# Kernel tuning notes

Measured on AMD Instinct MI355X. Metric: run time of the kernel, lower is better.

The kernel has to match this reference:

```python
import jax, jax.numpy as jnp
import numpy as np

N_NODES = 40000      # batch of group nodes
DEGREE = 32          # neighbors (members) per node
NUM_USERS = 100000
NUM_GROUPS = 50000
EMBED_DIM = 64


def setup_inputs() -> dict:
    key = jax.random.key(0)
    ks = jax.random.split(key, 8)
    E = N_NODES * DEGREE
    d = EMBED_DIM
    return {
        "nodes": jax.random.randint(ks[0], (N_NODES,), 0, NUM_GROUPS),
        "neigh_idx": jax.random.randint(ks[1], (E,), 0, NUM_USERS),
        # edge i belongs to node segment_ids[i]; sorted, DEGREE edges per node
        "segment_ids": jnp.repeat(jnp.arange(N_NODES), DEGREE),
        "u2e_weight": jax.random.normal(ks[2], (NUM_USERS, d), jnp.float32) * 0.02,
        "g2e_weight": jax.random.normal(ks[3], (NUM_GROUPS, d), jnp.float32) * 0.02,
        "att1_w": jax.random.normal(ks[4], (d, 2 * d), jnp.float32) * (1.0 / np.sqrt(2 * d)),
        "att1_b": jnp.zeros((d,), jnp.float32),
        "att2_w": jax.random.normal(ks[5], (d, d), jnp.float32) * (1.0 / np.sqrt(d)),
        "att2_b": jnp.zeros((d,), jnp.float32),
        "att3_w": jax.random.normal(ks[6], (1, d), jnp.float32) * (1.0 / np.sqrt(d)),
        "att3_b": jnp.zeros((1,), jnp.float32),
    }


def _segment_softmax(logits, seg, num_segments):
    # numerically stable softmax within each node's neighbor segment
    m = jax.ops.segment_max(logits, seg, num_segments=num_segments)
    a = jnp.exp(logits - m[seg])
    s = jax.ops.segment_sum(a, seg, num_segments=num_segments)
    return a / s[seg]


def reference(nodes, neigh_idx, segment_ids, u2e_weight, g2e_weight,
              att1_w, att1_b, att2_w, att2_b, att3_w, att3_b):
    e_u = u2e_weight[neigh_idx]                 # [E, d] member embeddings
    g_rep = g2e_weight[nodes][segment_ids]      # [E, d] group query broadcast per edge
    x = jnp.concatenate([e_u, g_rep], axis=-1)  # [E, 2d]
    h = jax.nn.relu(x @ att1_w.T + att1_b)      # [E, d] (dropout inactive at eval)
    h = jax.nn.relu(h @ att2_w.T + att2_b)      # [E, d]
    logits = (h @ att3_w.T + att3_b)[:, 0]      # [E]
    att = _segment_softmax(logits, segment_ids, N_NODES)  # [E]
    # attention-weighted aggregation of member embeddings per node
    return jax.ops.segment_sum(att[:, None] * e_u, segment_ids, num_segments=N_NODES)  # [N, d]
```

## Files before the change

### kernel.cpp

```cpp
#include <hip/hip_runtime.h>
#include <hip/hip_bf16.h>

typedef __attribute__((ext_vector_type(8))) short short8;
typedef __attribute__((ext_vector_type(4))) float floatx4;

#define NNODES 40000
#define NPW 4
#define WAVES 8
#define NPB (NPW * WAVES)
#define NBLK (NNODES / NPB)

#define U2E_ELEMS (100000 * 64)
#define WS_ALIGN 256
#define WS_NEEDED ((size_t)U2E_ELEMS * 2 + WS_ALIGN)


__device__ __forceinline__ float bf2f(unsigned short s) {
    return __uint_as_float(((unsigned int)s) << 16);
}
__device__ __forceinline__ unsigned short f2bf(float f) {
    unsigned int u = __float_as_uint(f);
    u += 0x7fffu + ((u >> 16) & 1u);
    return (unsigned short)(u >> 16);
}
__device__ __forceinline__ unsigned short f2bf_fast(float f) {
#if __has_builtin(__builtin_amdgcn_cvt_pk_bf16_f32)
    auto r = __builtin_amdgcn_cvt_pk_bf16_f32(f, f);
    unsigned int u; __builtin_memcpy(&u, &r, 4);
    return (unsigned short)u;
#else
    return f2bf(f);
#endif
}
__device__ __forceinline__ short8 cvt8(const float* fp) {
    floatx4 a = *(const floatx4*)fp;
    floatx4 b = *(const floatx4*)(fp + 4);
    short8 r;
    #pragma unroll
    for (int j = 0; j < 4; ++j) {
        r[j]     = (short)f2bf_fast(a[j]);
        r[4 + j] = (short)f2bf_fast(b[j]);
    }
    return r;
}

__global__ __launch_bounds__(256) void convert_u2e(
    const float* __restrict__ u2e, unsigned short* __restrict__ ub) {
    const size_t i = ((size_t)blockIdx.x * 256 + threadIdx.x) * 8;
    if (i < U2E_ELEMS) *(short8*)(ub + i) = cvt8(u2e + i);
}

template<int PRE>
__global__ __launch_bounds__(512, 4) void gat_fused(
    const int*   __restrict__ nodes,
    const int*   __restrict__ neigh,
    const float* __restrict__ u2f,
    const unsigned short* __restrict__ u2b,
    const float* __restrict__ g2e,
    const float* __restrict__ w1,
    const float* __restrict__ b1,
    const float* __restrict__ w2,
    const float* __restrict__ b2,
    const float* __restrict__ w3,
    float* __restrict__ out)
{
    __shared__ alignas(16) short w1f[16 * 64 * 8];
    __shared__ alignas(16) short w2f[8 * 64 * 8];
    __shared__ alignas(16) short hbuf[WAVES][32 * 72];

    const int tid  = threadIdx.x;
    const int wv   = tid >> 6;
    const int lane = tid & 63;
    const int q    = lane >> 4;
    const int n16  = lane & 15;

    for (int i = tid; i < 16 * 64; i += 512) {
        int s = i >> 6, slot = i & 63;
        int nt = s >> 2, kc = s & 3;
        int row = nt * 16 + (slot & 15);
        int k   = kc * 32 + (slot >> 4) * 8;
        *(short8*)&w1f[i * 8] = cvt8(w1 + (size_t)row * 128 + k);
    }
    for (int i = tid; i < 8 * 64; i += 512) {
        int s = i >> 6, slot = i & 63;
        int nt = s >> 1, kc = s & 1;
        int row = nt * 16 + (slot & 15);
        int k   = kc * 32 + (slot >> 4) * 8;
        *(short8*)&w2f[i * 8] = cvt8(w2 + (size_t)row * 64 + k);
    }
    float b1v[4], b2v[4], w3v[4];
    #pragma unroll
    for (int nt = 0; nt < 4; ++nt) {
        b1v[nt] = b1[nt * 16 + n16];
        b2v[nt] = b2[nt * 16 + n16];
        w3v[nt] = w3[nt * 16 + n16];
    }
    __syncthreads();

    const int n0 = blockIdx.x * NPB + wv * NPW;

    int gc, vc, c0, c1;
    int gn, vn, d0, d1;
    short8 A00, A01, A10, A11, G0, G1;

    auto loadA = [&](int idx, int half) -> short8 {
        if (PRE) return *(const short8*)(u2b + (size_t)idx * 64 + half * 32 + q * 8);
        else     return cvt8(u2f + (size_t)idx * 64 + half * 32 + q * 8);
    };

    {
        gc = nodes[n0];
        size_t eb = (size_t)n0 * 32;
        vc = neigh[eb + (lane & 31)];
        c0 = neigh[eb + n16];
        c1 = neigh[eb + 16 + n16];
        A00 = loadA(c0, 0); A01 = loadA(c0, 1);
        A10 = loadA(c1, 0); A11 = loadA(c1, 1);
        G0  = cvt8(g2e + (size_t)gc * 64 + q * 8);
        G1  = cvt8(g2e + (size_t)gc * 64 + 32 + q * 8);
        int n1 = n0 + 1;
        gn = nodes[n1];
        size_t eb1 = (size_t)n1 * 32;
        vn = neigh[eb1 + (lane & 31)];
        d0 = neigh[eb1 + n16];
        d1 = neigh[eb1 + 16 + n16];
    }

    const floatx4 zero4 = {0.f, 0.f, 0.f, 0.f};

    for (int it = 0; it < NPW; ++it) {
        const int n = n0 + it;
        const short8 a00 = A00, a01 = A01, a10 = A10, a11 = A11, g0 = G0, g1 = G1;
        const int idxv = vc;

        floatx4 acc[2][4];
        #pragma unroll
        for (int mt = 0; mt < 2; ++mt)
            #pragma unroll
            for (int nt = 0; nt < 4; ++nt) acc[mt][nt] = zero4;
        #pragma unroll
        for (int kc = 0; kc < 4; ++kc) {
            short8 x0 = (kc == 0) ? a00 : (kc == 1) ? a01 : (kc == 2) ? g0 : g1;
            short8 x1 = (kc == 0) ? a10 : (kc == 1) ? a11 : (kc == 2) ? g0 : g1;
            #pragma unroll
            for (int nt = 0; nt < 4; ++nt) {
                short8 b = *(const short8*)&w1f[((nt * 4 + kc) * 64 + lane) * 8];
                acc[0][nt] = __builtin_amdgcn_mfma_f32_16x16x32_bf16(x0, b, acc[0][nt], 0, 0, 0);
                acc[1][nt] = __builtin_amdgcn_mfma_f32_16x16x32_bf16(x1, b, acc[1][nt], 0, 0, 0);
            }
        }

        if (it < NPW - 1) {
            A00 = loadA(d0, 0); A01 = loadA(d0, 1);
            A10 = loadA(d1, 0); A11 = loadA(d1, 1);
            G0  = cvt8(g2e + (size_t)gn * 64 + q * 8);
            G1  = cvt8(g2e + (size_t)gn * 64 + 32 + q * 8);
            gc = gn; vc = vn; c0 = d0; c1 = d1;
            int nn = n0 + it + 2; if (nn > NNODES - 1) nn = NNODES - 1;
            gn = nodes[nn];
            size_t eb2 = (size_t)nn * 32;
            vn = neigh[eb2 + (lane & 31)];
            d0 = neigh[eb2 + n16];
            d1 = neigh[eb2 + 16 + n16];
        }

        __builtin_amdgcn_wave_barrier();
        #pragma unroll
        for (int mt = 0; mt < 2; ++mt)
            #pragma unroll
            for (int nt = 0; nt < 4; ++nt)
                #pragma unroll
                for (int r = 0; r < 4; ++r) {
                    float v = fmaxf(acc[mt][nt][r] + b1v[nt], 0.f);
                    hbuf[wv][(mt * 16 + q * 4 + r) * 72 + nt * 16 + n16] = (short)f2bf_fast(v);
                }
        __builtin_amdgcn_wave_barrier();

        short8 a2[2][2];
        #pragma unroll
        for (int mt = 0; mt < 2; ++mt)
            #pragma unroll
            for (int kc = 0; kc < 2; ++kc)
                a2[mt][kc] = *(const short8*)&hbuf[wv][(mt * 16 + n16) * 72 + kc * 32 + q * 8];

        floatx4 acc2[2][4];
        #pragma unroll
        for (int mt = 0; mt < 2; ++mt)
            #pragma unroll
            for (int nt = 0; nt < 4; ++nt) acc2[mt][nt] = zero4;
        #pragma unroll
        for (int kc = 0; kc < 2; ++kc)
            #pragma unroll
            for (int nt = 0; nt < 4; ++nt) {
                short8 b = *(const short8*)&w2f[((nt * 2 + kc) * 64 + lane) * 8];
                acc2[0][nt] = __builtin_amdgcn_mfma_f32_16x16x32_bf16(a2[0][kc], b, acc2[0][nt], 0, 0, 0);
                acc2[1][nt] = __builtin_amdgcn_mfma_f32_16x16x32_bf16(a2[1][kc], b, acc2[1][nt], 0, 0, 0);
            }

        float tt[2][4];
        #pragma unroll
        for (int mt = 0; mt < 2; ++mt)
            #pragma unroll
            for (int r = 0; r < 4; ++r) {
                float s = 0.f;
                #pragma unroll
                for (int nt = 0; nt < 4; ++nt)
                    s = fmaf(fmaxf(acc2[mt][nt][r] + b2v[nt], 0.f), w3v[nt], s);
                s += __shfl_xor(s, 1, 64);
                s += __shfl_xor(s, 2, 64);
                s += __shfl_xor(s, 4, 64);
                s += __shfl_xor(s, 8, 64);
                tt[mt][r] = s;
            }
        const int j = n16 & 7;
        float v0 = (j & 2) ? ((j & 1) ? tt[0][3] : tt[0][2]) : ((j & 1) ? tt[0][1] : tt[0][0]);
        float v1 = (j & 2) ? ((j & 1) ? tt[1][3] : tt[1][2]) : ((j & 1) ? tt[1][1] : tt[1][0]);
        float vm = (j & 4) ? v1 : v0;
        const int m = lane & 31;
        const int src = ((m & 12) << 2) | (((m >> 4) & 1) << 2) | (m & 3);
        const float lg = __shfl(vm, src, 64);

        float mx = lg;
        #pragma unroll
        for (int off = 1; off < 32; off <<= 1)
            mx = fmaxf(mx, __shfl_xor(mx, off, 64));
        const float ex = __expf(lg - mx);
        float sm = ex;
        #pragma unroll
        for (int off = 1; off < 32; off <<= 1)
            sm += __shfl_xor(sm, off, 64);
        const float attv = ex / sm;

        float acco = 0.f;
        #pragma unroll 16
        for (int e2 = 0; e2 < 32; ++e2) {
            int   sidx = __builtin_amdgcn_readlane(idxv, e2);
            float a    = __uint_as_float(__builtin_amdgcn_readlane(__float_as_uint(attv), e2));
            float ev   = PRE ? bf2f(u2b[(size_t)sidx * 64 + lane])
                             : u2f[(size_t)sidx * 64 + lane];
            acco = fmaf(a, ev, acco);
        }
        out[(size_t)n * 64 + lane] = acco;
    }
}

extern "C" void kernel_launch(void* const* d_in, const int* in_sizes, int n_in,
                              void* d_out, int out_size, void* d_ws, size_t ws_size,
                              hipStream_t stream) {
    const int*   nodes = (const int*)d_in[0];
    const int*   neigh = (const int*)d_in[1];
    const float* u2e = (const float*)d_in[3];
    const float* g2e = (const float*)d_in[4];
    const float* w1  = (const float*)d_in[5];
    const float* b1  = (const float*)d_in[6];
    const float* w2  = (const float*)d_in[7];
    const float* b2  = (const float*)d_in[8];
    const float* w3  = (const float*)d_in[9];
    float* out = (float*)d_out;

    if (ws_size >= WS_NEEDED) {
        unsigned short* ub = (unsigned short*)(((uintptr_t)d_ws + WS_ALIGN - 1) & ~(uintptr_t)(WS_ALIGN - 1));
        hipLaunchKernelGGL(convert_u2e, dim3((U2E_ELEMS / 8 + 255) / 256), dim3(256),
                           0, stream, u2e, ub);
        hipLaunchKernelGGL(gat_fused<1>, dim3(NBLK), dim3(512), 0, stream,
                           nodes, neigh, u2e, ub, g2e, w1, b1, w2, b2, w3, out);
    } else {
        hipLaunchKernelGGL(gat_fused<0>, dim3(NBLK), dim3(512), 0, stream,
                           nodes, neigh, u2e, (const unsigned short*)nullptr,
                           g2e, w1, b1, w2, b2, w3, out);
    }
}
```

Before: 177.1 us.

## Pre-convert group table to bf16 and halve per-wave LDS staging buffer

The conversion kernel now also turns the group embedding table into bf16 in the workspace, so the fused kernel reads group rows as bf16 instead of converting fp32 on every load. The per-wave hidden staging buffer shrinks from 72 to 40 columns by writing and reading the hidden activations in two halves, and the second-layer accumulators reuse the first-layer registers. The aim is less global traffic, lower LDS footprint and register pressure for better occupancy. The cost is converting the whole 50k-row group table each call (more than the 40k gathered rows), plus extra wave barriers.

Result: no change. 178.1 us (+0.6%).

```diff
diff --git a/kernel.cpp b/kernel.cpp
--- a/kernel.cpp
+++ b/kernel.cpp
@@ -11,8 +11,9 @@
 #define NBLK (NNODES / NPB)
 
 #define U2E_ELEMS (100000 * 64)
+#define G2E_ELEMS (50000 * 64)
 #define WS_ALIGN 256
-#define WS_NEEDED ((size_t)U2E_ELEMS * 2 + WS_ALIGN)
+#define WS_NEEDED (WS_ALIGN + (size_t)U2E_ELEMS * 2 + (size_t)G2E_ELEMS * 2)
 
 
 __device__ __forceinline__ float bf2f(unsigned short s) {
@@ -44,10 +45,12 @@
     return r;
 }
 
-__global__ __launch_bounds__(256) void convert_u2e(
-    const float* __restrict__ u2e, unsigned short* __restrict__ ub) {
+__global__ __launch_bounds__(256) void convert_tabs(
+    const float* __restrict__ u2e, const float* __restrict__ g2e,
+    unsigned short* __restrict__ ub, unsigned short* __restrict__ gb) {
     const size_t i = ((size_t)blockIdx.x * 256 + threadIdx.x) * 8;
     if (i < U2E_ELEMS) *(short8*)(ub + i) = cvt8(u2e + i);
+    if (i < G2E_ELEMS) *(short8*)(gb + i) = cvt8(g2e + i);
 }
 
 template<int PRE>
@@ -56,7 +59,8 @@
     const int*   __restrict__ neigh,
     const float* __restrict__ u2f,
     const unsigned short* __restrict__ u2b,
-    const float* __restrict__ g2e,
+    const float* __restrict__ g2f,
+    const unsigned short* __restrict__ g2b,
     const float* __restrict__ w1,
     const float* __restrict__ b1,
     const float* __restrict__ w2,
@@ -66,7 +70,7 @@
 {
     __shared__ alignas(16) short w1f[16 * 64 * 8];
     __shared__ alignas(16) short w2f[8 * 64 * 8];
-    __shared__ alignas(16) short hbuf[WAVES][32 * 72];
+    __shared__ alignas(16) short hbuf[WAVES][32 * 40];
 
     const int tid  = threadIdx.x;
     const int wv   = tid >> 6;
@@ -99,14 +103,18 @@
 
     const int n0 = blockIdx.x * NPB + wv * NPW;
 
-    int gc, vc, c0, c1;
-    int gn, vn, d0, d1;
-    short8 A00, A01, A10, A11, G0, G1;
-
     auto loadA = [&](int idx, int half) -> short8 {
         if (PRE) return *(const short8*)(u2b + (size_t)idx * 64 + half * 32 + q * 8);
         else     return cvt8(u2f + (size_t)idx * 64 + half * 32 + q * 8);
     };
+    auto loadG = [&](int idx, int half) -> short8 {
+        if (PRE) return *(const short8*)(g2b + (size_t)idx * 64 + half * 32 + q * 8);
+        else     return cvt8(g2f + (size_t)idx * 64 + half * 32 + q * 8);
+    };
+
+    int gc, vc, c0, c1;
+    int gn, vn, d0, d1;
+    short8 A00, A01, A10, A11, G0, G1;
 
     {
         gc = nodes[n0];
@@ -116,8 +124,7 @@
         c1 = neigh[eb + 16 + n16];
         A00 = loadA(c0, 0); A01 = loadA(c0, 1);
         A10 = loadA(c1, 0); A11 = loadA(c1, 1);
-        G0  = cvt8(g2e + (size_t)gc * 64 + q * 8);
-        G1  = cvt8(g2e + (size_t)gc * 64 + 32 + q * 8);
+        G0  = loadG(gc, 0); G1  = loadG(gc, 1);
         int n1 = n0 + 1;
         gn = nodes[n1];
         size_t eb1 = (size_t)n1 * 32;
@@ -153,8 +160,7 @@
         if (it < NPW - 1) {
             A00 = loadA(d0, 0); A01 = loadA(d0, 1);
             A10 = loadA(d1, 0); A11 = loadA(d1, 1);
-            G0  = cvt8(g2e + (size_t)gn * 64 + q * 8);
-            G1  = cvt8(g2e + (size_t)gn * 64 + 32 + q * 8);
+            G0  = loadG(gn, 0); G1  = loadG(gn, 1);
             gc = gn; vc = vn; c0 = d0; c1 = d1;
             int nn = n0 + it + 2; if (nn > NNODES - 1) nn = NNODES - 1;
             gn = nodes[nn];
@@ -164,37 +170,46 @@
             d1 = neigh[eb2 + 16 + n16];
         }
 
-        __builtin_amdgcn_wave_barrier();
-        #pragma unroll
-        for (int mt = 0; mt < 2; ++mt)
-            #pragma unroll
-            for (int nt = 0; nt < 4; ++nt)
+        short8 a2[2][2];
+        __builtin_amdgcn_wave_barrier();
+        #pragma unroll
+        for (int mt = 0; mt < 2; ++mt)
+            #pragma unroll
+            for (int nt = 0; nt < 2; ++nt)
                 #pragma unroll
                 for (int r = 0; r < 4; ++r) {
                     float v = fmaxf(acc[mt][nt][r] + b1v[nt], 0.f);
-                    hbuf[wv][(mt * 16 + q * 4 + r) * 72 + nt * 16 + n16] = (short)f2bf_fast(v);
+                    hbuf[wv][(mt * 16 + q * 4 + r) * 40 + nt * 16 + n16] = (short)f2bf_fast(v);
                 }
         __builtin_amdgcn_wave_barrier();
-
-        short8 a2[2][2];
-        #pragma unroll
-        for (int mt = 0; mt < 2; ++mt)
-            #pragma unroll
-            for (int kc = 0; kc < 2; ++kc)
-                a2[mt][kc] = *(const short8*)&hbuf[wv][(mt * 16 + n16) * 72 + kc * 32 + q * 8];
-
-        floatx4 acc2[2][4];
-        #pragma unroll
-        for (int mt = 0; mt < 2; ++mt)
-            #pragma unroll
-            for (int nt = 0; nt < 4; ++nt) acc2[mt][nt] = zero4;
+        a2[0][0] = *(const short8*)&hbuf[wv][(n16) * 40 + q * 8];
+        a2[1][0] = *(const short8*)&hbuf[wv][(16 + n16) * 40 + q * 8];
+        __builtin_amdgcn_wave_barrier();
+
+        #pragma unroll
+        for (int mt = 0; mt < 2; ++mt)
+            #pragma unroll
+            for (int nt = 2; nt < 4; ++nt)
+                #pragma unroll
+                for (int r = 0; r < 4; ++r) {
+                    float v = fmaxf(acc[mt][nt][r] + b1v[nt], 0.f);
+                    hbuf[wv][(mt * 16 + q * 4 + r) * 40 + (nt - 2) * 16 + n16] = (short)f2bf_fast(v);
+                }
+        __builtin_amdgcn_wave_barrier();
+        a2[0][1] = *(const short8*)&hbuf[wv][(n16) * 40 + q * 8];
+        a2[1][1] = *(const short8*)&hbuf[wv][(16 + n16) * 40 + q * 8];
+
+        #pragma unroll
+        for (int mt = 0; mt < 2; ++mt)
+            #pragma unroll
+            for (int nt = 0; nt < 4; ++nt) acc[mt][nt] = zero4;
         #pragma unroll
         for (int kc = 0; kc < 2; ++kc)
             #pragma unroll
             for (int nt = 0; nt < 4; ++nt) {
                 short8 b = *(const short8*)&w2f[((nt * 2 + kc) * 64 + lane) * 8];
-                acc2[0][nt] = __builtin_amdgcn_mfma_f32_16x16x32_bf16(a2[0][kc], b, acc2[0][nt], 0, 0, 0);
-                acc2[1][nt] = __builtin_amdgcn_mfma_f32_16x16x32_bf16(a2[1][kc], b, acc2[1][nt], 0, 0, 0);
+                acc[0][nt] = __builtin_amdgcn_mfma_f32_16x16x32_bf16(a2[0][kc], b, acc[0][nt], 0, 0, 0);
+                acc[1][nt] = __builtin_amdgcn_mfma_f32_16x16x32_bf16(a2[1][kc], b, acc[1][nt], 0, 0, 0);
             }
 
         float tt[2][4];
@@ -205,7 +220,7 @@
                 float s = 0.f;
                 #pragma unroll
                 for (int nt = 0; nt < 4; ++nt)
-                    s = fmaf(fmaxf(acc2[mt][nt][r] + b2v[nt], 0.f), w3v[nt], s);
+                    s = fmaf(fmaxf(acc[mt][nt][r] + b2v[nt], 0.f), w3v[nt], s);
                 s += __shfl_xor(s, 1, 64);
                 s += __shfl_xor(s, 2, 64);
                 s += __shfl_xor(s, 4, 64);
@@ -260,13 +275,15 @@
 
     if (ws_size >= WS_NEEDED) {
         unsigned short* ub = (unsigned short*)(((uintptr_t)d_ws + WS_ALIGN - 1) & ~(uintptr_t)(WS_ALIGN - 1));
-        hipLaunchKernelGGL(convert_u2e, dim3((U2E_ELEMS / 8 + 255) / 256), dim3(256),
-                           0, stream, u2e, ub);
+        unsigned short* gb = ub + U2E_ELEMS;
+        hipLaunchKernelGGL(convert_tabs, dim3((U2E_ELEMS / 8 + 255) / 256), dim3(256),
+                           0, stream, u2e, g2e, ub, gb);
         hipLaunchKernelGGL(gat_fused<1>, dim3(NBLK), dim3(512), 0, stream,
-                           nodes, neigh, u2e, ub, g2e, w1, b1, w2, b2, w3, out);
+                           nodes, neigh, u2e, ub, g2e, gb, w1, b1, w2, b2, w3, out);
     } else {
         hipLaunchKernelGGL(gat_fused<0>, dim3(NBLK), dim3(512), 0, stream,
                            nodes, neigh, u2e, (const unsigned short*)nullptr,
-                           g2e, w1, b1, w2, b2, w3, out);
-    }
-}
+                           g2e, (const unsigned short*)nullptr,
+                           w1, b1, w2, b2, w3, out);
+    }
+}
```
